# Kernel optimization log

Hardware: AMD Instinct MI355X
Metric: run time of the kernel (lower is better)

Reference implementation:

```python
import jax, jax.numpy as jnp
import numpy as np

K = 4          # knn (loop=True -> self included as nearest)
NEG_SLOPE = 0.2  # PyG GATConv leaky_relu slope


def knn_neighbors(coords, k=K):
    """coords: [B, P, 2] -> global neighbor indices [B*P, k].
    Per-batch brute-force kNN (cdist + top_k), sequential over batch to
    bound the [P, P] distance matrix memory, matching torch_cluster.knn_graph
    with loop=True and a per-image batch vector."""
    B, P, _ = coords.shape

    def per_batch(c):  # c: [P, 2]
        d = jnp.sum((c[:, None, :] - c[None, :, :]) ** 2, axis=-1)  # [P, P]
        _, idx = jax.lax.top_k(-d, k)  # self (dist 0) is included -> loop=True
        return idx

    idx = jax.lax.map(per_batch, coords)  # [B, P, k], local indices
    offs = (jnp.arange(B, dtype=idx.dtype) * P)[:, None, None]
    return (idx + offs).reshape(B * P, k)  # global node ids


def gat_layer(x, nbr, W, a_src, a_dst, b, concat):
    """PyG GATConv (eval mode, dropout off) on a fixed-degree kNN graph.
    x: [N, Cin], nbr: [N, k] source nodes j for each target i.
    alpha_ij = softmax_j leaky_relu(a_src.h_j + a_dst.h_i); out_i = sum_j alpha_ij h_j."""
    H, F = a_src.shape
    h = (x @ W).reshape(-1, H, F)                      # [N, H, F]
    asrc = jnp.einsum('nhf,hf->nh', h, a_src)          # [N, H]
    adst = jnp.einsum('nhf,hf->nh', h, a_dst)          # [N, H]
    e = jax.nn.leaky_relu(asrc[nbr] + adst[:, None, :], NEG_SLOPE)  # [N, k, H]
    alpha = jax.nn.softmax(e, axis=1)                  # softmax over neighbors
    out = jnp.einsum('nkh,nkhf->nhf', alpha, h[nbr])   # [N, H, F]
    if concat:
        out = out.reshape(-1, H * F)
    else:
        out = out.mean(axis=1)                         # heads=1 -> identity
    return out + b


def gat_forward(coords, x, W0, att_src0, att_dst0, b0, W1, att_src1, att_dst1, b1,
                W2, att_src2, att_dst2, b2):
    B, P, _ = coords.shape
    nbr = knn_neighbors(coords)
    h = gat_layer(x, nbr, W0, att_src0, att_dst0, b0, concat=True)
    h = jax.nn.elu(h)
    h = gat_layer(h, nbr, W1, att_src1, att_dst1, b1, concat=True)
    h = jax.nn.elu(h)
    h = gat_layer(h, nbr, W2, att_src2, att_dst2, b2, concat=False)
    return h.reshape(B, P, -1)  # pred_logits [B, P, num_classes+1]


def setup_inputs() -> dict:
    key = jax.random.key(0)
    ks = jax.random.split(key, 16)
    B, P, N = 16, 8192, 16 * 8192
    s = 0.05
    return {
        'coords': jax.random.uniform(ks[0], (B, P, 2), dtype=jnp.float32),
        'x': jax.random.normal(ks[1], (N, 256), dtype=jnp.float32),
        'W0': jax.random.normal(ks[2], (256, 256), dtype=jnp.float32) * s,
        'att_src0': jax.random.normal(ks[3], (4, 64), dtype=jnp.float32) * s,
        'att_dst0': jax.random.normal(ks[4], (4, 64), dtype=jnp.float32) * s,
        'b0': jax.random.normal(ks[5], (256,), dtype=jnp.float32) * s,
        'W1': jax.random.normal(ks[6], (256, 256), dtype=jnp.float32) * s,
        'att_src1': jax.random.normal(ks[7], (4, 64), dtype=jnp.float32) * s,
        'att_dst1': jax.random.normal(ks[8], (4, 64), dtype=jnp.float32) * s,
        'b1': jax.random.normal(ks[9], (256,), dtype=jnp.float32) * s,
        'W2': jax.random.normal(ks[10], (256, 2), dtype=jnp.float32) * s,
        'att_src2': jax.random.normal(ks[11], (1, 2), dtype=jnp.float32) * s,
        'att_dst2': jax.random.normal(ks[12], (1, 2), dtype=jnp.float32) * s,
        'b2': jax.random.normal(ks[13], (2,), dtype=jnp.float32) * s,
    }


def reference(coords, x, W0, att_src0, att_dst0, b0, W1, att_src1, att_dst1, b1,
              W2, att_src2, att_dst2, b2):
    return gat_forward(coords, x, W0, att_src0, att_dst0, b0,
                       W1, att_src1, att_dst1, b1, W2, att_src2, att_dst2, b2)
```

## Files before the change

kernel.cpp:

```cpp
#include <hip/hip_runtime.h>
#include <math.h>

constexpr int Bn = 16, Pn = 8192, Nn = 16 * 8192;
constexpr int GB = 32;
constexpr int NBIN = GB * GB;

typedef __attribute__((ext_vector_type(8))) short short8;
typedef __attribute__((ext_vector_type(4))) float f32x4;

__device__ __forceinline__ unsigned short f2bf(float f) {
  unsigned u = __builtin_bit_cast(unsigned, f);
  unsigned r = (u + 0x7FFFu + ((u >> 16) & 1u)) >> 16;
  return (unsigned short)r;
}
__device__ __forceinline__ float bf2f(unsigned short h) {
  unsigned u = ((unsigned)h) << 16;
  return __builtin_bit_cast(float, u);
}

__global__ __launch_bounds__(256) void bin_count(const float* __restrict__ coords,
                                                 int* __restrict__ counts) {
  const int n = blockIdx.x * 256 + threadIdx.x;
  const int b = n >> 13;
  float2 c = ((const float2*)coords)[n];
  int bx = min(GB - 1, (int)(c.x * (float)GB));
  int by = min(GB - 1, (int)(c.y * (float)GB));
  atomicAdd(&counts[b * NBIN + by * GB + bx], 1);
}

__global__ __launch_bounds__(1024) void bin_scan(const int* __restrict__ counts,
                                                 int* __restrict__ starts,
                                                 int* __restrict__ cursor) {
  __shared__ int s[NBIN];
  const int b = blockIdx.x, t = threadIdx.x;
  const int v = counts[b * NBIN + t];
  s[t] = v;
  __syncthreads();
  for (int off = 1; off < NBIN; off <<= 1) {
    int x = (t >= off) ? s[t - off] : 0;
    __syncthreads();
    s[t] += x;
    __syncthreads();
  }
  const int excl = s[t] - v;
  starts[b * NBIN + t] = excl;
  cursor[b * NBIN + t] = excl;
}

__global__ __launch_bounds__(256) void bin_scatter(const float* __restrict__ coords,
                                                   int* __restrict__ cursor,
                                                   float2* __restrict__ pts,
                                                   int* __restrict__ ids) {
  const int n = blockIdx.x * 256 + threadIdx.x;
  const int b = n >> 13, p = n & (Pn - 1);
  float2 c = ((const float2*)coords)[n];
  int bx = min(GB - 1, (int)(c.x * (float)GB));
  int by = min(GB - 1, (int)(c.y * (float)GB));
  int slot = atomicAdd(&cursor[b * NBIN + by * GB + bx], 1);
  pts[(size_t)b * Pn + slot] = c;
  ids[(size_t)b * Pn + slot] = p;
}

__global__ __launch_bounds__(256) void knn_query(const float* __restrict__ coords,
                                                 const int* __restrict__ starts,
                                                 const int* __restrict__ counts,
                                                 const float2* __restrict__ pts,
                                                 const int* __restrict__ ids,
                                                 int* __restrict__ nbr) {
  const int n = blockIdx.x * 256 + threadIdx.x;
  const int b = n >> 13;
  const float2 q = ((const float2*)coords)[n];
  const float qx = q.x, qy = q.y;
  const float w = 1.0f / (float)GB;
  const int bx = min(GB - 1, (int)(qx * (float)GB));
  const int by = min(GB - 1, (int)(qy * (float)GB));
  const float2* bp = pts + (size_t)b * Pn;
  const int* bi = ids + (size_t)b * Pn;
  const int* bs = starts + b * NBIN;
  const int* bc = counts + b * NBIN;

  float d0v = 3.4e38f, d1v = 3.4e38f, d2v = 3.4e38f, d3v = 3.4e38f;
  int i0v = 0x7fffffff, i1v = 0x7fffffff, i2v = 0x7fffffff, i3v = 0x7fffffff;

#define LLT(da, ia, db, ib) ((da) < (db) || ((da) == (db) && (ia) < (ib)))
#define LEX_INSERT(dd, jj)                                              \
  if (LLT(dd, jj, d3v, i3v)) {                                          \
    if (LLT(dd, jj, d2v, i2v)) {                                        \
      d3v = d2v; i3v = i2v;                                             \
      if (LLT(dd, jj, d1v, i1v)) {                                      \
        d2v = d1v; i2v = i1v;                                           \
        if (LLT(dd, jj, d0v, i0v)) { d1v = d0v; i1v = i0v; d0v = dd; i0v = jj; } \
        else { d1v = dd; i1v = jj; }                                    \
      } else { d2v = dd; i2v = jj; }                                    \
    } else { d3v = dd; i3v = jj; }                                      \
  }
#define SCAN_CELL(xx, yy)                                               \
  {                                                                     \
    const int cell = (yy) * GB + (xx);                                  \
    const int s0 = bs[cell], cnt = bc[cell];                            \
    for (int s = s0; s < s0 + cnt; ++s) {                               \
      float2 pp = bp[s];                                                \
      int jj = bi[s];                                                   \
      float dx = qx - pp.x, dy = qy - pp.y;                             \
      float dd = __fadd_rn(__fmul_rn(dx, dx), __fmul_rn(dy, dy));       \
      LEX_INSERT(dd, jj);                                               \
    }                                                                   \
  }

  for (int k = 0; k < GB; ++k) {
    const int xlo = bx - k, xhi = bx + k, ylo = by - k, yhi = by + k;
    const int cxlo = max(0, xlo), cxhi = min(GB - 1, xhi);
    const int cylo = max(0, ylo), cyhi = min(GB - 1, yhi);
    for (int yy = cylo; yy <= cyhi; ++yy) {
      const bool edge = (yy == ylo) || (yy == yhi);
      if (edge || k == 0) {
        for (int xx = cxlo; xx <= cxhi; ++xx) SCAN_CELL(xx, yy);
      } else {
        if (xlo >= 0) SCAN_CELL(xlo, yy);
        if (xhi <= GB - 1) SCAN_CELL(xhi, yy);
      }
    }
    float m = 1e30f;
    bool open = false;
    if (xlo > 0)      { m = fminf(m, qx - (float)xlo * w); open = true; }
    if (xhi < GB - 1) { m = fminf(m, (float)(xhi + 1) * w - qx); open = true; }
    if (ylo > 0)      { m = fminf(m, qy - (float)ylo * w); open = true; }
    if (yhi < GB - 1) { m = fminf(m, (float)(yhi + 1) * w - qy); open = true; }
    if (!open) break;
    m -= 1e-6f;
    if (d3v < 3.0e38f && m > 0.f && __fmul_rn(m, m) >= d3v) break;
  }
#undef SCAN_CELL
#undef LEX_INSERT
#undef LLT

  const int base = b * Pn;
  *(int4*)&nbr[(size_t)n * 4] =
      make_int4(base + i0v, base + i1v, base + i2v, base + i3v);
}

__global__ __launch_bounds__(256) void wt_kernel(const float* __restrict__ W,
                                                 unsigned short* __restrict__ Wth,
                                                 unsigned short* __restrict__ Wtl) {
  const int k = blockIdx.x, n = threadIdx.x;
  float v = W[k * 256 + n];
  unsigned short h = f2bf(v);
  unsigned short l = f2bf(v - bf2f(h));
  Wth[n * 256 + k] = h;
  Wtl[n * 256 + k] = l;
}

__global__ __launch_bounds__(256, 2) void gemm_bf3(const float* __restrict__ A,
                                                   const unsigned short* __restrict__ Bth,
                                                   const unsigned short* __restrict__ Btl,
                                                   float* __restrict__ C) {
  __shared__ unsigned short Ah[128][40], Al[128][40];
  __shared__ unsigned short Bh[128][40], Bl[128][40];
  const int t = threadIdx.x;
  const int row0 = blockIdx.y * 128;
  const int col0 = blockIdx.x * 128;
  const int wid = t >> 6, lane = t & 63;
  const int wr = (wid >> 1) * 64, wc = (wid & 1) * 64;
  const int lrow = lane & 15, lko = (lane >> 4) * 8;

  f32x4 acc[4][4];
#pragma unroll
  for (int i = 0; i < 4; ++i)
#pragma unroll
    for (int j = 0; j < 4; ++j) acc[i][j] = {0.f, 0.f, 0.f, 0.f};

  for (int kt = 0; kt < 8; ++kt) {
    const int k0 = kt * 32;
    float4 av[4];
#pragma unroll
    for (int i = 0; i < 4; ++i) {
      const int idx = t + i * 256;
      const int row = idx >> 3, kq = idx & 7;
      av[i] = *(const float4*)&A[(size_t)(row0 + row) * 256 + k0 + kq * 4];
    }
    uint4 bh[2], bl[2];
#pragma unroll
    for (int i = 0; i < 2; ++i) {
      const int idx = t + i * 256;
      const int col = idx >> 2, kc = idx & 3;
      bh[i] = *(const uint4*)&Bth[(size_t)(col0 + col) * 256 + k0 + kc * 8];
      bl[i] = *(const uint4*)&Btl[(size_t)(col0 + col) * 256 + k0 + kc * 8];
    }
    __syncthreads();
#pragma unroll
    for (int i = 0; i < 4; ++i) {
      const int idx = t + i * 256;
      const int row = idx >> 3, kq = idx & 7;
      const float vv[4] = {av[i].x, av[i].y, av[i].z, av[i].w};
      unsigned short hh[4], ll[4];
#pragma unroll
      for (int e = 0; e < 4; ++e) {
        hh[e] = f2bf(vv[e]);
        ll[e] = f2bf(vv[e] - bf2f(hh[e]));
      }
      *(ushort4*)&Ah[row][kq * 4] = make_ushort4(hh[0], hh[1], hh[2], hh[3]);
      *(ushort4*)&Al[row][kq * 4] = make_ushort4(ll[0], ll[1], ll[2], ll[3]);
    }
#pragma unroll
    for (int i = 0; i < 2; ++i) {
      const int idx = t + i * 256;
      const int col = idx >> 2, kc = idx & 3;
      *(uint4*)&Bh[col][kc * 8] = bh[i];
      *(uint4*)&Bl[col][kc * 8] = bl[i];
    }
    __syncthreads();
    short8 afh[4], afl[4], bfh[4], bfl[4];
#pragma unroll
    for (int f = 0; f < 4; ++f) {
      afh[f] = *(const short8*)&Ah[wr + f * 16 + lrow][lko];
      afl[f] = *(const short8*)&Al[wr + f * 16 + lrow][lko];
      bfh[f] = *(const short8*)&Bh[wc + f * 16 + lrow][lko];
      bfl[f] = *(const short8*)&Bl[wc + f * 16 + lrow][lko];
    }
#pragma unroll
    for (int fr = 0; fr < 4; ++fr)
#pragma unroll
      for (int fc = 0; fc < 4; ++fc) {
        acc[fr][fc] = __builtin_amdgcn_mfma_f32_16x16x32_bf16(afh[fr], bfh[fc], acc[fr][fc], 0, 0, 0);
        acc[fr][fc] = __builtin_amdgcn_mfma_f32_16x16x32_bf16(afh[fr], bfl[fc], acc[fr][fc], 0, 0, 0);
        acc[fr][fc] = __builtin_amdgcn_mfma_f32_16x16x32_bf16(afl[fr], bfh[fc], acc[fr][fc], 0, 0, 0);
      }
  }
#pragma unroll
  for (int fr = 0; fr < 4; ++fr)
#pragma unroll
    for (int fc = 0; fc < 4; ++fc) {
      const int col = col0 + wc + fc * 16 + (lane & 15);
#pragma unroll
      for (int j = 0; j < 4; ++j) {
        const int row = row0 + wr + fr * 16 + (lane >> 4) * 4 + j;
        C[(size_t)row * 256 + col] = acc[fr][fc][j];
      }
    }
}

__global__ __launch_bounds__(256) void attn_coeff_kernel(const float* __restrict__ g,
                                                         const float* __restrict__ att_src,
                                                         const float* __restrict__ att_dst,
                                                         float* __restrict__ asrc,
                                                         float* __restrict__ adst) {
  const int t = threadIdx.x;
  const int lane = t & 63;
  const int n = blockIdx.x * 4 + (t >> 6);
  float4 v  = *(const float4*)&g[(size_t)n * 256 + lane * 4];
  float4 as = *(const float4*)&att_src[lane * 4];
  float4 ad = *(const float4*)&att_dst[lane * 4];
  float ps = v.x * as.x + v.y * as.y + v.z * as.z + v.w * as.w;
  float pd = v.x * ad.x + v.y * ad.y + v.z * ad.z + v.w * ad.w;
#pragma unroll
  for (int off = 1; off < 16; off <<= 1) {
    ps += __shfl_xor(ps, off);
    pd += __shfl_xor(pd, off);
  }
  if ((lane & 15) == 0) {
    asrc[(size_t)n * 4 + (lane >> 4)] = ps;
    adst[(size_t)n * 4 + (lane >> 4)] = pd;
  }
}

__device__ __forceinline__ float leaky02(float x) { return x >= 0.f ? x : 0.2f * x; }

__global__ __launch_bounds__(256) void aggregate_fused(const float* __restrict__ g,
                                                       const int* __restrict__ nbr,
                                                       const float* __restrict__ asrc,
                                                       const float* __restrict__ adst,
                                                       const float* __restrict__ bias,
                                                       float* __restrict__ y) {
  const int t = threadIdx.x;
  const int lane = t & 63;
  const int n = blockIdx.x * 4 + (t >> 6);
  int4 nb = *(const int4*)&nbr[(size_t)n * 4];
  const int h = lane >> 4;
  const float adh = adst[(size_t)n * 4 + h];
  float e0 = leaky02(asrc[(size_t)nb.x * 4 + h] + adh);
  float e1 = leaky02(asrc[(size_t)nb.y * 4 + h] + adh);
  float e2 = leaky02(asrc[(size_t)nb.z * 4 + h] + adh);
  float e3 = leaky02(asrc[(size_t)nb.w * 4 + h] + adh);
  float m = fmaxf(fmaxf(fmaxf(e0, e1), e2), e3);
  float x0 = expf(e0 - m), x1 = expf(e1 - m), x2 = expf(e2 - m), x3 = expf(e3 - m);
  float s = ((x0 + x1) + x2) + x3;
  const float a0 = x0 / s, a1 = x1 / s, a2 = x2 / s, a3 = x3 / s;

  const int c = lane * 4;
  float4 v0 = *(const float4*)&g[(size_t)nb.x * 256 + c];
  float4 v1 = *(const float4*)&g[(size_t)nb.y * 256 + c];
  float4 v2 = *(const float4*)&g[(size_t)nb.z * 256 + c];
  float4 v3 = *(const float4*)&g[(size_t)nb.w * 256 + c];
  float4 bb = *(const float4*)&bias[c];
  float4 o;
  o.x = a0 * v0.x + a1 * v1.x + a2 * v2.x + a3 * v3.x + bb.x;
  o.y = a0 * v0.y + a1 * v1.y + a2 * v2.y + a3 * v3.y + bb.y;
  o.z = a0 * v0.z + a1 * v1.z + a2 * v2.z + a3 * v3.z + bb.z;
  o.w = a0 * v0.w + a1 * v1.w + a2 * v2.w + a3 * v3.w + bb.w;
  o.x = o.x > 0.f ? o.x : expm1f(o.x);
  o.y = o.y > 0.f ? o.y : expm1f(o.y);
  o.z = o.z > 0.f ? o.z : expm1f(o.z);
  o.w = o.w > 0.f ? o.w : expm1f(o.w);
  *(float4*)&y[(size_t)n * 256 + c] = o;
}

__global__ __launch_bounds__(256) void aggregate_h2(const float* __restrict__ g,
                                                    const int* __restrict__ nbr,
                                                    const float* __restrict__ asrc,
                                                    const float* __restrict__ adst,
                                                    const float* __restrict__ bias,
                                                    const float* __restrict__ W2,
                                                    const float* __restrict__ as2,
                                                    const float* __restrict__ ad2,
                                                    float* __restrict__ g2,
                                                    float* __restrict__ asrc2,
                                                    float* __restrict__ adst2) {
  const int t = threadIdx.x;
  const int lane = t & 63;
  const int n = blockIdx.x * 4 + (t >> 6);
  int4 nb = *(const int4*)&nbr[(size_t)n * 4];
  const int h = lane >> 4;
  const float adh = adst[(size_t)n * 4 + h];
  float e0 = leaky02(asrc[(size_t)nb.x * 4 + h] + adh);
  float e1 = leaky02(asrc[(size_t)nb.y * 4 + h] + adh);
  float e2 = leaky02(asrc[(size_t)nb.z * 4 + h] + adh);
  float e3 = leaky02(asrc[(size_t)nb.w * 4 + h] + adh);
  float m = fmaxf(fmaxf(fmaxf(e0, e1), e2), e3);
  float x0 = expf(e0 - m), x1 = expf(e1 - m), x2 = expf(e2 - m), x3 = expf(e3 - m);
  float s = ((x0 + x1) + x2) + x3;
  const float a0 = x0 / s, a1 = x1 / s, a2 = x2 / s, a3 = x3 / s;

  const int c = lane * 4;
  float4 v0 = *(const float4*)&g[(size_t)nb.x * 256 + c];
  float4 v1 = *(const float4*)&g[(size_t)nb.y * 256 + c];
  float4 v2 = *(const float4*)&g[(size_t)nb.z * 256 + c];
  float4 v3 = *(const float4*)&g[(size_t)nb.w * 256 + c];
  float4 bb = *(const float4*)&bias[c];
  float4 o;
  o.x = a0 * v0.x + a1 * v1.x + a2 * v2.x + a3 * v3.x + bb.x;
  o.y = a0 * v0.y + a1 * v1.y + a2 * v2.y + a3 * v3.y + bb.y;
  o.z = a0 * v0.z + a1 * v1.z + a2 * v2.z + a3 * v3.z + bb.z;
  o.w = a0 * v0.w + a1 * v1.w + a2 * v2.w + a3 * v3.w + bb.w;
  o.x = o.x > 0.f ? o.x : expm1f(o.x);
  o.y = o.y > 0.f ? o.y : expm1f(o.y);
  o.z = o.z > 0.f ? o.z : expm1f(o.z);
  o.w = o.w > 0.f ? o.w : expm1f(o.w);

  const float w00 = W2[(c + 0) * 2 + 0], w01 = W2[(c + 0) * 2 + 1];
  const float w10 = W2[(c + 1) * 2 + 0], w11 = W2[(c + 1) * 2 + 1];
  const float w20 = W2[(c + 2) * 2 + 0], w21 = W2[(c + 2) * 2 + 1];
  const float w30 = W2[(c + 3) * 2 + 0], w31 = W2[(c + 3) * 2 + 1];
  float p0 = o.x * w00 + o.y * w10 + o.z * w20 + o.w * w30;
  float p1 = o.x * w01 + o.y * w11 + o.z * w21 + o.w * w31;
#pragma unroll
  for (int off = 1; off < 64; off <<= 1) {
    p0 += __shfl_xor(p0, off);
    p1 += __shfl_xor(p1, off);
  }
  if (lane == 0) {
    g2[(size_t)n * 2]     = p0;
    g2[(size_t)n * 2 + 1] = p1;
    asrc2[n] = p0 * as2[0] + p1 * as2[1];
    adst2[n] = p0 * ad2[0] + p1 * ad2[1];
  }
}

__global__ __launch_bounds__(256) void final_kernel(const int* __restrict__ nbr,
                                                    const float* __restrict__ g2,
                                                    const float* __restrict__ asrc2,
                                                    const float* __restrict__ adst2,
                                                    const float* __restrict__ b2,
                                                    float* __restrict__ out) {
  const int n = blockIdx.x * 256 + threadIdx.x;
  int4 nb = *(const int4*)&nbr[(size_t)n * 4];
  const float ad = adst2[n];
  float e0 = leaky02(asrc2[nb.x] + ad);
  float e1 = leaky02(asrc2[nb.y] + ad);
  float e2 = leaky02(asrc2[nb.z] + ad);
  float e3 = leaky02(asrc2[nb.w] + ad);
  float m = fmaxf(fmaxf(e0, e1), fmaxf(e2, e3));
  float x0 = expf(e0 - m), x1 = expf(e1 - m), x2 = expf(e2 - m), x3 = expf(e3 - m);
  float s = x0 + x1 + x2 + x3;
  float o0 = (x0 * g2[(size_t)nb.x * 2] + x1 * g2[(size_t)nb.y * 2] +
              x2 * g2[(size_t)nb.z * 2] + x3 * g2[(size_t)nb.w * 2]) / s;
  float o1 = (x0 * g2[(size_t)nb.x * 2 + 1] + x1 * g2[(size_t)nb.y * 2 + 1] +
              x2 * g2[(size_t)nb.z * 2 + 1] + x3 * g2[(size_t)nb.w * 2 + 1]) / s;
  out[(size_t)n * 2]     = o0 + b2[0];
  out[(size_t)n * 2 + 1] = o1 + b2[1];
}

extern "C" void kernel_launch(void* const* d_in, const int* in_sizes, int n_in,
                              void* d_out, int out_size, void* d_ws, size_t ws_size,
                              hipStream_t stream) {
  const float* coords = (const float*)d_in[0];
  const float* x   = (const float*)d_in[1];
  const float* W0  = (const float*)d_in[2];
  const float* as0 = (const float*)d_in[3];
  const float* ad0 = (const float*)d_in[4];
  const float* b0  = (const float*)d_in[5];
  const float* W1  = (const float*)d_in[6];
  const float* as1 = (const float*)d_in[7];
  const float* ad1 = (const float*)d_in[8];
  const float* b1  = (const float*)d_in[9];
  const float* W2  = (const float*)d_in[10];
  const float* as2 = (const float*)d_in[11];
  const float* ad2 = (const float*)d_in[12];
  const float* b2  = (const float*)d_in[13];
  float* out = (float*)d_out;

  float* g     = (float*)d_ws;
  float* y     = g + (size_t)Nn * 256;
  int*   nbr   = (int*)(y + (size_t)Nn * 256);
  float* asrc  = (float*)(nbr + (size_t)Nn * 4);
  float* adst  = asrc + (size_t)Nn * 4;
  float* g2    = adst + (size_t)Nn * 4;
  float* s2    = g2 + (size_t)Nn * 2;
  float* d2    = s2 + (size_t)Nn;
  unsigned short* Wth = (unsigned short*)(d2 + (size_t)Nn);
  unsigned short* Wtl = Wth + 256 * 256;
  float2* pts  = (float2*)(Wtl + 256 * 256);
  int* ids     = (int*)(pts + (size_t)Bn * Pn);
  int* counts  = ids + (size_t)Bn * Pn;
  int* starts  = counts + Bn * NBIN;
  int* cursor  = starts + Bn * NBIN;

  hipMemsetAsync(counts, 0, Bn * NBIN * sizeof(int), stream);
  bin_count<<<Nn / 256, 256, 0, stream>>>(coords, counts);
  bin_scan<<<Bn, NBIN, 0, stream>>>(counts, starts, cursor);
  bin_scatter<<<Nn / 256, 256, 0, stream>>>(coords, cursor, pts, ids);
  knn_query<<<Nn / 256, 256, 0, stream>>>(coords, starts, counts, pts, ids, nbr);

  wt_kernel<<<256, 256, 0, stream>>>(W0, Wth, Wtl);
  gemm_bf3<<<dim3(2, Nn / 128), 256, 0, stream>>>(x, Wth, Wtl, g);
  attn_coeff_kernel<<<Nn / 4, 256, 0, stream>>>(g, as0, ad0, asrc, adst);
  aggregate_fused<<<Nn / 4, 256, 0, stream>>>(g, nbr, asrc, adst, b0, y);

  wt_kernel<<<256, 256, 0, stream>>>(W1, Wth, Wtl);
  gemm_bf3<<<dim3(2, Nn / 128), 256, 0, stream>>>(y, Wth, Wtl, g);
  attn_coeff_kernel<<<Nn / 4, 256, 0, stream>>>(g, as1, ad1, asrc, adst);
  aggregate_h2<<<Nn / 4, 256, 0, stream>>>(g, nbr, asrc, adst, b1, W2, as2, ad2,
                                           g2, s2, d2);

  final_kernel<<<Nn / 256, 256, 0, stream>>>(nbr, g2, s2, d2, b2, out);
}
```

Before: 733.1 us.

## Fuse attention coefficients into GEMM epilogue and prefetch next K tile

Folds the per-node attention dot products (asrc/adst) into the bf16x3 GEMM epilogue, using the accumulator registers plus a cross-lane reduction, and removes the separate attn_coeff kernel that re-read the full 256-wide feature matrix. The GEMM main loop now issues global loads for the next K tile after the shared-memory stores, so they overlap with the MFMA work. LDS row padding shrinks from 40 to 36 and the launch-bounds occupancy hint rises from 2 to 3 blocks. The prefetch and the fused epilogue raise register pressure, and the new padding may change LDS bank conflicts.

Result: faster. 706.7 us (-3.6%).

```diff
diff --git a/kernel.cpp b/kernel.cpp
--- a/kernel.cpp
+++ b/kernel.cpp
@@ -150,12 +150,16 @@
   Wtl[n * 256 + k] = l;
 }
 
-__global__ __launch_bounds__(256, 2) void gemm_bf3(const float* __restrict__ A,
+__global__ __launch_bounds__(256, 3) void gemm_bf3(const float* __restrict__ A,
                                                    const unsigned short* __restrict__ Bth,
                                                    const unsigned short* __restrict__ Btl,
-                                                   float* __restrict__ C) {
-  __shared__ unsigned short Ah[128][40], Al[128][40];
-  __shared__ unsigned short Bh[128][40], Bl[128][40];
+                                                   const float* __restrict__ att_src,
+                                                   const float* __restrict__ att_dst,
+                                                   float* __restrict__ C,
+                                                   float* __restrict__ asrc,
+                                                   float* __restrict__ adst) {
+  __shared__ unsigned short Ah[128][36], Al[128][36];
+  __shared__ unsigned short Bh[128][36], Bl[128][36];
   const int t = threadIdx.x;
   const int row0 = blockIdx.y * 128;
   const int col0 = blockIdx.x * 128;
@@ -169,23 +173,29 @@
 #pragma unroll
     for (int j = 0; j < 4; ++j) acc[i][j] = {0.f, 0.f, 0.f, 0.f};
 
+  float4 av[4];
+  uint4 bhv[2], blv[2];
+
+#define GLOAD(ktv)                                                          \
+  {                                                                         \
+    const int k0 = (ktv) * 32;                                              \
+    _Pragma("unroll")                                                       \
+    for (int i = 0; i < 4; ++i) {                                           \
+      const int idx = t + i * 256;                                          \
+      const int row = idx >> 3, kq = idx & 7;                               \
+      av[i] = *(const float4*)&A[(size_t)(row0 + row) * 256 + k0 + kq * 4]; \
+    }                                                                       \
+    _Pragma("unroll")                                                       \
+    for (int i = 0; i < 2; ++i) {                                           \
+      const int idx = t + i * 256;                                          \
+      const int col = idx >> 2, kc = idx & 3;                               \
+      bhv[i] = *(const uint4*)&Bth[(size_t)(col0 + col) * 256 + k0 + kc * 8]; \
+      blv[i] = *(const uint4*)&Btl[(size_t)(col0 + col) * 256 + k0 + kc * 8]; \
+    }                                                                       \
+  }
+
+  GLOAD(0);
   for (int kt = 0; kt < 8; ++kt) {
-    const int k0 = kt * 32;
-    float4 av[4];
-#pragma unroll
-    for (int i = 0; i < 4; ++i) {
-      const int idx = t + i * 256;
-      const int row = idx >> 3, kq = idx & 7;
-      av[i] = *(const float4*)&A[(size_t)(row0 + row) * 256 + k0 + kq * 4];
-    }
-    uint4 bh[2], bl[2];
-#pragma unroll
-    for (int i = 0; i < 2; ++i) {
-      const int idx = t + i * 256;
-      const int col = idx >> 2, kc = idx & 3;
-      bh[i] = *(const uint4*)&Bth[(size_t)(col0 + col) * 256 + k0 + kc * 8];
-      bl[i] = *(const uint4*)&Btl[(size_t)(col0 + col) * 256 + k0 + kc * 8];
-    }
     __syncthreads();
 #pragma unroll
     for (int i = 0; i < 4; ++i) {
@@ -205,10 +215,11 @@
     for (int i = 0; i < 2; ++i) {
       const int idx = t + i * 256;
       const int col = idx >> 2, kc = idx & 3;
-      *(uint4*)&Bh[col][kc * 8] = bh[i];
-      *(uint4*)&Bl[col][kc * 8] = bl[i];
+      *(uint4*)&Bh[col][kc * 8] = bhv[i];
+      *(uint4*)&Bl[col][kc * 8] = blv[i];
     }
     __syncthreads();
+    if (kt < 7) GLOAD(kt + 1);
     short8 afh[4], afl[4], bfh[4], bfl[4];
 #pragma unroll
     for (int f = 0; f < 4; ++f) {
@@ -226,41 +237,48 @@
         acc[fr][fc] = __builtin_amdgcn_mfma_f32_16x16x32_bf16(afl[fr], bfh[fc], acc[fr][fc], 0, 0, 0);
       }
   }
+#undef GLOAD
+
 #pragma unroll
   for (int fr = 0; fr < 4; ++fr)
 #pragma unroll
     for (int fc = 0; fc < 4; ++fc) {
-      const int col = col0 + wc + fc * 16 + (lane & 15);
+      const int col = col0 + wc + fc * 16 + lrow;
 #pragma unroll
       for (int j = 0; j < 4; ++j) {
         const int row = row0 + wr + fr * 16 + (lane >> 4) * 4 + j;
         C[(size_t)row * 256 + col] = acc[fr][fc][j];
       }
     }
-}
-
-__global__ __launch_bounds__(256) void attn_coeff_kernel(const float* __restrict__ g,
-                                                         const float* __restrict__ att_src,
-                                                         const float* __restrict__ att_dst,
-                                                         float* __restrict__ asrc,
-                                                         float* __restrict__ adst) {
-  const int t = threadIdx.x;
-  const int lane = t & 63;
-  const int n = blockIdx.x * 4 + (t >> 6);
-  float4 v  = *(const float4*)&g[(size_t)n * 256 + lane * 4];
-  float4 as = *(const float4*)&att_src[lane * 4];
-  float4 ad = *(const float4*)&att_dst[lane * 4];
-  float ps = v.x * as.x + v.y * as.y + v.z * as.z + v.w * as.w;
-  float pd = v.x * ad.x + v.y * ad.y + v.z * ad.z + v.w * ad.w;
-#pragma unroll
-  for (int off = 1; off < 16; off <<= 1) {
-    ps += __shfl_xor(ps, off);
-    pd += __shfl_xor(pd, off);
-  }
-  if ((lane & 15) == 0) {
-    asrc[(size_t)n * 4 + (lane >> 4)] = ps;
-    adst[(size_t)n * 4 + (lane >> 4)] = pd;
-  }
+
+  const int h = (col0 >> 6) + (wid & 1);
+  float asv[4], adv[4];
+#pragma unroll
+  for (int fc = 0; fc < 4; ++fc) {
+    asv[fc] = att_src[h * 64 + fc * 16 + lrow];
+    adv[fc] = att_dst[h * 64 + fc * 16 + lrow];
+  }
+#pragma unroll
+  for (int fr = 0; fr < 4; ++fr)
+#pragma unroll
+    for (int j = 0; j < 4; ++j) {
+      float ps = 0.f, pd = 0.f;
+#pragma unroll
+      for (int fc = 0; fc < 4; ++fc) {
+        ps += acc[fr][fc][j] * asv[fc];
+        pd += acc[fr][fc][j] * adv[fc];
+      }
+#pragma unroll
+      for (int off = 1; off < 16; off <<= 1) {
+        ps += __shfl_xor(ps, off);
+        pd += __shfl_xor(pd, off);
+      }
+      if (lrow == 0) {
+        const int row = row0 + wr + fr * 16 + (lane >> 4) * 4 + j;
+        asrc[(size_t)row * 4 + h] = ps;
+        adst[(size_t)row * 4 + h] = pd;
+      }
+    }
 }
 
 __device__ __forceinline__ float leaky02(float x) { return x >= 0.f ? x : 0.2f * x; }
@@ -431,13 +449,11 @@
   knn_query<<<Nn / 256, 256, 0, stream>>>(coords, starts, counts, pts, ids, nbr);
 
   wt_kernel<<<256, 256, 0, stream>>>(W0, Wth, Wtl);
-  gemm_bf3<<<dim3(2, Nn / 128), 256, 0, stream>>>(x, Wth, Wtl, g);
-  attn_coeff_kernel<<<Nn / 4, 256, 0, stream>>>(g, as0, ad0, asrc, adst);
+  gemm_bf3<<<dim3(2, Nn / 128), 256, 0, stream>>>(x, Wth, Wtl, as0, ad0, g, asrc, adst);
   aggregate_fused<<<Nn / 4, 256, 0, stream>>>(g, nbr, asrc, adst, b0, y);
 
   wt_kernel<<<256, 256, 0, stream>>>(W1, Wth, Wtl);
-  gemm_bf3<<<dim3(2, Nn / 128), 256, 0, stream>>>(y, Wth, Wtl, g);
-  attn_coeff_kernel<<<Nn / 4, 256, 0, stream>>>(g, as1, ad1, asrc, adst);
+  gemm_bf3<<<dim3(2, Nn / 128), 256, 0, stream>>>(y, Wth, Wtl, as1, ad1, g, asrc, adst);
   aggregate_h2<<<Nn / 4, 256, 0, stream>>>(g, nbr, asrc, adst, b1, W2, as2, ad2,
                                            g2, s2, d2);
 
```
